# Performance work log

Measured on AMD Instinct MI355X. Metric: run time of the kernel, lower is better.

The kernel has to match this reference:

```python
import jax, jax.numpy as jnp
import numpy as np

B, Q, C, V = 512, 100, 81, 117  # batch, queries, obj classes (80+no-object), verbs
THRES, ALPHA, BETA = 0.7, 1.0, 0.5


def setup_inputs() -> dict:
    key = jax.random.key(0)
    k1, k2, k3, k4, k5, k6 = jax.random.split(key, 6)
    out_obj_logits = jax.random.normal(k1, (B, Q, C), jnp.float32)
    out_verb_logits = jax.random.normal(k2, (B, Q, V), jnp.float32)
    out_sub_boxes = jax.random.uniform(k3, (B, Q, 4), jnp.float32)
    out_obj_boxes = jax.random.uniform(k4, (B, Q, 4), jnp.float32)
    # correct_mat: binary verb-object compatibility [V, C-1] + ones column for no-object slot -> [V, C]
    cm = (jax.random.uniform(k5, (V, C - 1)) < 0.3).astype(jnp.float32)
    correct_mat = jnp.concatenate([cm, jnp.ones((V, 1), jnp.float32)], axis=1)
    target_sizes = jax.random.randint(k6, (B, 2), 480, 1334).astype(jnp.int64)
    return {
        'out_obj_logits': out_obj_logits,
        'out_verb_logits': out_verb_logits,
        'out_sub_boxes': out_sub_boxes,
        'out_obj_boxes': out_obj_boxes,
        'correct_mat': correct_mat,
        'target_sizes': target_sizes,
    }


def _box_cxcywh_to_xyxy(b):
    cx, cy, w, h = b[..., 0], b[..., 1], b[..., 2], b[..., 3]
    return jnp.stack([cx - 0.5 * w, cy - 0.5 * h, cx + 0.5 * w, cy + 0.5 * h], axis=-1)


def _pairwise_iou(boxes):  # boxes [Q,4] xyxy (pixel coords, +1 convention as in source)
    x1, y1, x2, y2 = boxes[:, 0], boxes[:, 1], boxes[:, 2], boxes[:, 3]
    area = (x2 - x1 + 1.0) * (y2 - y1 + 1.0)
    xx1 = jnp.maximum(x1[:, None], x1[None, :])
    yy1 = jnp.maximum(y1[:, None], y1[None, :])
    xx2 = jnp.minimum(x2[:, None], x2[None, :])
    yy2 = jnp.minimum(y2[:, None], y2[None, :])
    w = jnp.maximum(0.0, xx2 - xx1 + 1.0)
    h = jnp.maximum(0.0, yy2 - yy1 + 1.0)
    inter = w * h
    union = area[:, None] + area[None, :] - inter
    return inter / union


def _nms_one_image(sub_b, obj_b, obj_lab, max_scores):
    # Greedy pairwise triplet NMS. Grouping key in the source degenerates to the
    # object label alone (subject cat is constant, verb-label string identical),
    # so suppression applies only between detections with the same object label.
    order = jnp.argsort(-max_scores)
    sb, ob, lab = sub_b[order], obj_b[order], obj_lab[order]
    ovr = jnp.power(_pairwise_iou(sb), ALPHA) * jnp.power(_pairwise_iou(ob), BETA)
    upper = jnp.triu(jnp.ones((Q, Q), bool), 1)
    sup_mat = upper & (lab[:, None] == lab[None, :]) & (ovr > THRES)

    def body(i, supp):
        return supp | (sup_mat[i] & jnp.logical_not(supp[i]))

    supp = jax.lax.fori_loop(0, Q, body, jnp.zeros((Q,), bool))
    keep = jnp.zeros((Q,), bool).at[order].set(jnp.logical_not(supp))
    return keep  # in original query order


def reference(out_obj_logits, out_verb_logits, out_sub_boxes, out_obj_boxes, correct_mat, target_sizes):
    obj_prob = jax.nn.softmax(out_obj_logits, axis=-1)
    obj_scores = obj_prob[..., :-1].max(axis=-1)            # [B,Q]
    obj_labels = obj_prob[..., :-1].argmax(axis=-1)         # [B,Q]
    verb_scores = jax.nn.sigmoid(out_verb_logits)           # [B,Q,V]

    ts = target_sizes.astype(jnp.float32)
    img_h, img_w = ts[:, 0], ts[:, 1]
    scale_fct = jnp.stack([img_w, img_h, img_w, img_h], axis=1)  # [B,4]
    sub_boxes = _box_cxcywh_to_xyxy(out_sub_boxes) * scale_fct[:, None, :]
    obj_boxes = _box_cxcywh_to_xyxy(out_obj_boxes) * scale_fct[:, None, :]

    # masks[b,q,v] = correct_mat[v, obj_labels[b,q]]
    masks = correct_mat.T[obj_labels]                        # [B,Q,V]
    hoi_scores = verb_scores * obj_scores[..., None] * masks

    max_scores = hoi_scores.max(axis=-1)                     # [B,Q]
    keep = jax.vmap(_nms_one_image)(sub_boxes, obj_boxes, obj_labels, max_scores)
    return hoi_scores, obj_labels, sub_boxes, obj_boxes, keep
```

## Files before the change

### kernel.cpp

```cpp
#include <hip/hip_runtime.h>
#include <math.h>

#define Bn 512
#define Qn 100
#define Cn 81
#define Vn 117
#define NQ (Bn * Qn)

#define OFF_HOI  0
#define OFF_LAB  (NQ * Vn)
#define OFF_SUB  (OFF_LAB + NQ)
#define OFF_OBJ  (OFF_SUB + NQ * 4)
#define OFF_KEEP (OFF_OBJ + NQ * 4)

__device__ __forceinline__ float frcp(float x) { return __builtin_amdgcn_rcpf(x); }

__global__ __launch_bounds__(256) void hoi_fused(
    const float* __restrict__ obj_logits,
    const float* __restrict__ verb_logits,
    const float* __restrict__ sub_boxes,
    const float* __restrict__ obj_boxes,
    const float* __restrict__ cm,
    const int*   __restrict__ target_sizes,
    float* __restrict__ out)
{
    __shared__ float CM[Vn * Cn];
    __shared__ float L[16 * Cn];
    __shared__ float W[16 * Vn];
    __shared__ float sc[Qn];
    __shared__ int   labs[Qn];
    __shared__ float4 Bsub[Qn], Bobj[Qn];
    __shared__ float4 Ssub[Qn], Sobj[Qn], Smeta[Qn];
    __shared__ unsigned long long RR[2 * Qn];

    const int tid = threadIdx.x;
    const int b   = blockIdx.x;
    const int t   = tid & 15;
    const int g   = tid >> 4;

    {
        const float4* c4 = (const float4*)cm;
        float4* C4 = (float4*)CM;
        for (int i = tid; i < (Vn * Cn) / 4; i += 256) C4[i] = c4[i];
        if (tid == 0) CM[Vn * Cn - 1] = cm[Vn * Cn - 1];
    }

    const float ih = (float)target_sizes[2 * b + 0];
    const float iw = (float)target_sizes[2 * b + 1];

    if (tid < Qn) {
        const int idx = b * Qn + tid;
        float4 bx = ((const float4*)sub_boxes)[idx];
        float4 r;
        r.x = (bx.x - 0.5f * bx.z) * iw;
        r.y = (bx.y - 0.5f * bx.w) * ih;
        r.z = (bx.x + 0.5f * bx.z) * iw;
        r.w = (bx.y + 0.5f * bx.w) * ih;
        ((float4*)(out + OFF_SUB))[idx] = r;
        Bsub[tid] = r;
        bx = ((const float4*)obj_boxes)[idx];
        r.x = (bx.x - 0.5f * bx.z) * iw;
        r.y = (bx.y - 0.5f * bx.w) * ih;
        r.z = (bx.x + 0.5f * bx.z) * iw;
        r.w = (bx.y + 0.5f * bx.w) * ih;
        ((float4*)(out + OFF_OBJ))[idx] = r;
        Bobj[tid] = r;
    }

    for (int p = 0; p < 7; p++) {
        const int q0  = p * 16;
        const int cnt = (q0 + 16 <= Qn) ? 16 : (Qn - q0);

        {
            const float4* lgs = (const float4*)(obj_logits + ((size_t)b * Qn + q0) * Cn);
            float4* Lv = (float4*)L;
            const int nL = cnt * Cn / 4;
            for (int i = tid; i < nL; i += 256) Lv[i] = lgs[i];
            const float4* vls = (const float4*)(verb_logits + ((size_t)b * Qn + q0) * Vn);
            float4* Wv = (float4*)W;
            const int nW = cnt * Vn / 4;
            for (int i = tid; i < nW; i += 256) Wv[i] = vls[i];
        }
        __syncthreads();

        if (g < cnt) {
            const int q   = q0 + g;
            const int idx = b * Qn + q;

            const float* lg = L + g * Cn;
            float l0 = lg[t], l1 = lg[t + 16], l2 = lg[t + 32], l3 = lg[t + 48], l4 = lg[t + 64];
            float l5 = lg[80];

            float v = l0; int vid = t;
            if (l1 > v) { v = l1; vid = t + 16; }
            if (l2 > v) { v = l2; vid = t + 32; }
            if (l3 > v) { v = l3; vid = t + 48; }
            if (l4 > v) { v = l4; vid = t + 64; }
            #pragma unroll
            for (int o = 8; o; o >>= 1) {
                float ov = __shfl_xor(v, o, 64);
                int   oi = __shfl_xor(vid, o, 64);
                if (ov > v || (ov == v && oi < vid)) { v = ov; vid = oi; }
            }

            float e = __expf(l0) + __expf(l1) + __expf(l2) + __expf(l3) + __expf(l4);
            #pragma unroll
            for (int o = 8; o; o >>= 1) e += __shfl_xor(e, o, 64);
            e += __expf(l5);

            const int   label     = vid;
            const float obj_score = __expf(v) * frcp(e);

            float* vrow = W + g * Vn;
            float mx = 0.f;
            #pragma unroll
            for (int c = 0; c < 8; c++) {
                int col = t + 16 * c;
                if (col < Vn) {
                    float x = vrow[col];
                    float h = frcp(1.f + __expf(-x)) * obj_score * CM[col * Cn + label];
                    vrow[col] = h;
                    mx = fmaxf(mx, h);
                }
            }
            #pragma unroll
            for (int o = 8; o; o >>= 1) mx = fmaxf(mx, __shfl_xor(mx, o, 64));

            if (t == 0) {
                out[OFF_LAB + idx] = (float)label;
                sc[q]   = mx;
                labs[q] = label;
            }
        }
        __syncthreads();

        {
            const float4* Wv = (const float4*)W;
            float4* ho = (float4*)(out + OFF_HOI + ((size_t)b * Qn + q0) * Vn);
            const int nW = cnt * Vn / 4;
            for (int i = tid; i < nW; i += 256) ho[i] = Wv[i];
        }
        __syncthreads();
    }

    if (tid < Qn) {
        const float kv = sc[tid];
        int r = 0;
        #pragma unroll 4
        for (int j = 0; j < Qn; j++) {
            float sj = sc[j];
            r += (sj > kv) || (sj == kv && j < tid);
        }
        float4 sb = Bsub[tid], ob = Bobj[tid];
        Ssub[r] = sb;
        Sobj[r] = ob;
        Smeta[r] = make_float4((sb.z - sb.x + 1.f) * (sb.w - sb.y + 1.f),
                               (ob.z - ob.x + 1.f) * (ob.w - ob.y + 1.f),
                               (float)labs[tid], (float)tid);
    }
    __syncthreads();

    {
        const int tc   = tid & 127;
        const int half = tid >> 7;
        const int lane = tid & 63;
        const int sub  = (tid >> 6) & 1;
        const bool jv  = (tc < Qn);

        float4 js = make_float4(0.f, 0.f, 0.f, 0.f), jo = js, jm = js;
        if (jv) { js = Ssub[tc]; jo = Sobj[tc]; jm = Smeta[tc]; }

        const int i0 = half ? 50 : 0;
        const int i1 = half ? (Qn - 1) : 50;
        for (int i = i0; i < i1; i++) {
            float4 is = Ssub[i], io = Sobj[i], im = Smeta[i];
            float ww = fmaxf(0.f, fminf(is.z, js.z) - fmaxf(is.x, js.x) + 1.f);
            float hh = fmaxf(0.f, fminf(is.w, js.w) - fmaxf(is.y, js.y) + 1.f);
            float inter = ww * hh;
            float iou_s = inter / (im.x + jm.x - inter);
            ww = fmaxf(0.f, fminf(io.z, jo.z) - fmaxf(io.x, jo.x) + 1.f);
            hh = fmaxf(0.f, fminf(io.w, jo.w) - fmaxf(io.y, jo.y) + 1.f);
            inter = ww * hh;
            float iou_o = inter / (im.y + jm.y - inter);
            bool cond = jv && (tc > i) && (jm.z == im.z) && (iou_s * sqrtf(iou_o) > 0.7f);
            unsigned long long m = __ballot(cond);
            if (lane == 0) RR[2 * i + sub] = m;
        }
    }
    __syncthreads();

    if (tid < 64) {
        unsigned long long s0 = 0ull, s1 = 0ull;
        for (int k = 0; k < Qn - 1; k++) {
            unsigned long long dead = ((k < 64 ? s0 : s1) >> (k & 63)) & 1ull;
            if (!dead) { s0 |= RR[2 * k]; s1 |= RR[2 * k + 1]; }
        }
        float* keepp = out + OFF_KEEP + (size_t)b * Qn;
        keepp[(int)Smeta[tid].w] = ((s0 >> tid) & 1ull) ? 0.f : 1.f;
        if (tid < 36)
            keepp[(int)Smeta[64 + tid].w] = ((s1 >> tid) & 1ull) ? 0.f : 1.f;
    }
}

extern "C" void kernel_launch(void* const* d_in, const int* in_sizes, int n_in,
                              void* d_out, int out_size, void* d_ws, size_t ws_size,
                              hipStream_t stream) {
    const float* obj_logits   = (const float*)d_in[0];
    const float* verb_logits  = (const float*)d_in[1];
    const float* sub_boxes    = (const float*)d_in[2];
    const float* obj_boxes    = (const float*)d_in[3];
    const float* correct_mat  = (const float*)d_in[4];
    const int*   target_sizes = (const int*)d_in[5];
    float* out = (float*)d_out;
    (void)d_ws; (void)ws_size; (void)in_sizes; (void)n_in; (void)out_size;

    hoi_fused<<<Bn, 256, 0, stream>>>(obj_logits, verb_logits, sub_boxes,
                                      obj_boxes, correct_mat, target_sizes, out);
}
```

Baseline: 140.3 us.

## Read logits directly from global, drop LDS staging, use 512 threads and alias LDS

```diff
diff --git a/kernel.cpp b/kernel.cpp
--- a/kernel.cpp
+++ b/kernel.cpp
@@ -15,7 +15,7 @@
 
 __device__ __forceinline__ float frcp(float x) { return __builtin_amdgcn_rcpf(x); }
 
-__global__ __launch_bounds__(256) void hoi_fused(
+__global__ __launch_bounds__(512) void hoi_fused(
     const float* __restrict__ obj_logits,
     const float* __restrict__ verb_logits,
     const float* __restrict__ sub_boxes,
@@ -24,72 +24,59 @@
     const int*   __restrict__ target_sizes,
     float* __restrict__ out)
 {
-    __shared__ float CM[Vn * Cn];
-    __shared__ float L[16 * Cn];
-    __shared__ float W[16 * Vn];
+    __shared__ __align__(16) char smem[37920];
     __shared__ float sc[Qn];
     __shared__ int   labs[Qn];
-    __shared__ float4 Bsub[Qn], Bobj[Qn];
-    __shared__ float4 Ssub[Qn], Sobj[Qn], Smeta[Qn];
-    __shared__ unsigned long long RR[2 * Qn];
+
+    float*      CM    = (float*)smem;
+    float4*     Ssub  = (float4*)smem;
+    float4*     Sobj  = Ssub + Qn;
+    float4*     Smeta = Sobj + Qn;
+    ulonglong2* RR    = (ulonglong2*)(Smeta + Qn);
 
     const int tid = threadIdx.x;
     const int b   = blockIdx.x;
-    const int t   = tid & 15;
-    const int g   = tid >> 4;
 
     {
         const float4* c4 = (const float4*)cm;
         float4* C4 = (float4*)CM;
-        for (int i = tid; i < (Vn * Cn) / 4; i += 256) C4[i] = c4[i];
+        for (int i = tid; i < (Vn * Cn) / 4; i += 512) C4[i] = c4[i];
         if (tid == 0) CM[Vn * Cn - 1] = cm[Vn * Cn - 1];
     }
 
-    const float ih = (float)target_sizes[2 * b + 0];
-    const float iw = (float)target_sizes[2 * b + 1];
-
+    float4 rs = make_float4(0.f, 0.f, 0.f, 0.f), ro = rs;
     if (tid < Qn) {
+        const float ih = (float)target_sizes[2 * b + 0];
+        const float iw = (float)target_sizes[2 * b + 1];
         const int idx = b * Qn + tid;
         float4 bx = ((const float4*)sub_boxes)[idx];
-        float4 r;
-        r.x = (bx.x - 0.5f * bx.z) * iw;
-        r.y = (bx.y - 0.5f * bx.w) * ih;
-        r.z = (bx.x + 0.5f * bx.z) * iw;
-        r.w = (bx.y + 0.5f * bx.w) * ih;
-        ((float4*)(out + OFF_SUB))[idx] = r;
-        Bsub[tid] = r;
+        rs.x = (bx.x - 0.5f * bx.z) * iw;
+        rs.y = (bx.y - 0.5f * bx.w) * ih;
+        rs.z = (bx.x + 0.5f * bx.z) * iw;
+        rs.w = (bx.y + 0.5f * bx.w) * ih;
+        ((float4*)(out + OFF_SUB))[idx] = rs;
         bx = ((const float4*)obj_boxes)[idx];
-        r.x = (bx.x - 0.5f * bx.z) * iw;
-        r.y = (bx.y - 0.5f * bx.w) * ih;
-        r.z = (bx.x + 0.5f * bx.z) * iw;
-        r.w = (bx.y + 0.5f * bx.w) * ih;
-        ((float4*)(out + OFF_OBJ))[idx] = r;
-        Bobj[tid] = r;
-    }
-
-    for (int p = 0; p < 7; p++) {
-        const int q0  = p * 16;
-        const int cnt = (q0 + 16 <= Qn) ? 16 : (Qn - q0);
-
-        {
-            const float4* lgs = (const float4*)(obj_logits + ((size_t)b * Qn + q0) * Cn);
-            float4* Lv = (float4*)L;
-            const int nL = cnt * Cn / 4;
-            for (int i = tid; i < nL; i += 256) Lv[i] = lgs[i];
-            const float4* vls = (const float4*)(verb_logits + ((size_t)b * Qn + q0) * Vn);
-            float4* Wv = (float4*)W;
-            const int nW = cnt * Vn / 4;
-            for (int i = tid; i < nW; i += 256) Wv[i] = vls[i];
-        }
-        __syncthreads();
-
-        if (g < cnt) {
-            const int q   = q0 + g;
-            const int idx = b * Qn + q;
-
-            const float* lg = L + g * Cn;
-            float l0 = lg[t], l1 = lg[t + 16], l2 = lg[t + 32], l3 = lg[t + 48], l4 = lg[t + 64];
-            float l5 = lg[80];
+        ro.x = (bx.x - 0.5f * bx.z) * iw;
+        ro.y = (bx.y - 0.5f * bx.w) * ih;
+        ro.z = (bx.x + 0.5f * bx.z) * iw;
+        ro.w = (bx.y + 0.5f * bx.w) * ih;
+        ((float4*)(out + OFF_OBJ))[idx] = ro;
+    }
+    __syncthreads();
+
+    {
+        const int t = tid & 15;
+        const int g = tid >> 4;
+        for (int q = g; q < Qn; q += 32) {
+            const size_t idx = (size_t)b * Qn + q;
+            const float* lg = obj_logits + idx * Cn;
+            const float* vl = verb_logits + idx * Vn;
+
+            float l0 = lg[t], l1 = lg[t + 16], l2 = lg[t + 32],
+                  l3 = lg[t + 48], l4 = lg[t + 64], l5 = lg[80];
+            float w0 = vl[t], w1 = vl[t + 16], w2 = vl[t + 32], w3 = vl[t + 48],
+                  w4 = vl[t + 64], w5 = vl[t + 80], w6 = vl[t + 96];
+            float w7 = (t < 5) ? vl[112 + t] : 0.f;
 
             float v = l0; int vid = t;
             if (l1 > v) { v = l1; vid = t + 16; }
@@ -111,16 +98,28 @@
             const int   label     = vid;
             const float obj_score = __expf(v) * frcp(e);
 
-            float* vrow = W + g * Vn;
+            float* hout = out + OFF_HOI + idx * Vn;
+            const float* cmrow = CM + label;
             float mx = 0.f;
-            #pragma unroll
-            for (int c = 0; c < 8; c++) {
-                int col = t + 16 * c;
-                if (col < Vn) {
-                    float x = vrow[col];
-                    float h = frcp(1.f + __expf(-x)) * obj_score * CM[col * Cn + label];
-                    vrow[col] = h;
-                    mx = fmaxf(mx, h);
+            {
+                float h;
+                h = frcp(1.f + __expf(-w0)) * obj_score * cmrow[(t      ) * Cn];
+                hout[t      ] = h; mx = fmaxf(mx, h);
+                h = frcp(1.f + __expf(-w1)) * obj_score * cmrow[(t +  16) * Cn];
+                hout[t +  16] = h; mx = fmaxf(mx, h);
+                h = frcp(1.f + __expf(-w2)) * obj_score * cmrow[(t +  32) * Cn];
+                hout[t +  32] = h; mx = fmaxf(mx, h);
+                h = frcp(1.f + __expf(-w3)) * obj_score * cmrow[(t +  48) * Cn];
+                hout[t +  48] = h; mx = fmaxf(mx, h);
+                h = frcp(1.f + __expf(-w4)) * obj_score * cmrow[(t +  64) * Cn];
+                hout[t +  64] = h; mx = fmaxf(mx, h);
+                h = frcp(1.f + __expf(-w5)) * obj_score * cmrow[(t +  80) * Cn];
+                hout[t +  80] = h; mx = fmaxf(mx, h);
+                h = frcp(1.f + __expf(-w6)) * obj_score * cmrow[(t +  96) * Cn];
+                hout[t +  96] = h; mx = fmaxf(mx, h);
+                if (t < 5) {
+                    h = frcp(1.f + __expf(-w7)) * obj_score * cmrow[(112 + t) * Cn];
+                    hout[112 + t] = h; mx = fmaxf(mx, h);
                 }
             }
             #pragma unroll
@@ -132,16 +131,8 @@
                 labs[q] = label;
             }
         }
-        __syncthreads();
-
-        {
-            const float4* Wv = (const float4*)W;
-            float4* ho = (float4*)(out + OFF_HOI + ((size_t)b * Qn + q0) * Vn);
-            const int nW = cnt * Vn / 4;
-            for (int i = tid; i < nW; i += 256) ho[i] = Wv[i];
-        }
-        __syncthreads();
-    }
+    }
+    __syncthreads();
 
     if (tid < Qn) {
         const float kv = sc[tid];
@@ -151,18 +142,17 @@
             float sj = sc[j];
             r += (sj > kv) || (sj == kv && j < tid);
         }
-        float4 sb = Bsub[tid], ob = Bobj[tid];
-        Ssub[r] = sb;
-        Sobj[r] = ob;
-        Smeta[r] = make_float4((sb.z - sb.x + 1.f) * (sb.w - sb.y + 1.f),
-                               (ob.z - ob.x + 1.f) * (ob.w - ob.y + 1.f),
+        Ssub[r] = rs;
+        Sobj[r] = ro;
+        Smeta[r] = make_float4((rs.z - rs.x + 1.f) * (rs.w - rs.y + 1.f),
+                               (ro.z - ro.x + 1.f) * (ro.w - ro.y + 1.f),
                                (float)labs[tid], (float)tid);
     }
     __syncthreads();
 
     {
         const int tc   = tid & 127;
-        const int half = tid >> 7;
+        const int uq   = tid >> 7;
         const int lane = tid & 63;
         const int sub  = (tid >> 6) & 1;
         const bool jv  = (tc < Qn);
@@ -170,8 +160,8 @@
         float4 js = make_float4(0.f, 0.f, 0.f, 0.f), jo = js, jm = js;
         if (jv) { js = Ssub[tc]; jo = Sobj[tc]; jm = Smeta[tc]; }
 
-        const int i0 = half ? 50 : 0;
-        const int i1 = half ? (Qn - 1) : 50;
+        const int i0 = 25 * uq;
+        const int i1 = (25 * uq + 25 < Qn - 1) ? 25 * uq + 25 : Qn - 1;
         for (int i = i0; i < i1; i++) {
             float4 is = Ssub[i], io = Sobj[i], im = Smeta[i];
             float ww = fmaxf(0.f, fminf(is.z, js.z) - fmaxf(is.x, js.x) + 1.f);
@@ -184,16 +174,19 @@
             float iou_o = inter / (im.y + jm.y - inter);
             bool cond = jv && (tc > i) && (jm.z == im.z) && (iou_s * sqrtf(iou_o) > 0.7f);
             unsigned long long m = __ballot(cond);
-            if (lane == 0) RR[2 * i + sub] = m;
+            if (lane == 0) ((unsigned long long*)&RR[i])[sub] = m;
         }
     }
     __syncthreads();
 
     if (tid < 64) {
         unsigned long long s0 = 0ull, s1 = 0ull;
+        ulonglong2 r = RR[0];
         for (int k = 0; k < Qn - 1; k++) {
+            ulonglong2 rn = RR[(k + 1 < Qn - 1) ? k + 1 : k];
             unsigned long long dead = ((k < 64 ? s0 : s1) >> (k & 63)) & 1ull;
-            if (!dead) { s0 |= RR[2 * k]; s1 |= RR[2 * k + 1]; }
+            if (!dead) { s0 |= r.x; s1 |= r.y; }
+            r = rn;
         }
         float* keepp = out + OFF_KEEP + (size_t)b * Qn;
         keepp[(int)Smeta[tid].w] = ((s0 >> tid) & 1ull) ? 0.f : 1.f;
@@ -214,6 +207,6 @@
     float* out = (float*)d_out;
     (void)d_ws; (void)ws_size; (void)in_sizes; (void)n_in; (void)out_size;
 
-    hoi_fused<<<Bn, 256, 0, stream>>>(obj_logits, verb_logits, sub_boxes,
+    hoi_fused<<<Bn, 512, 0, stream>>>(obj_logits, verb_logits, sub_boxes,
                                       obj_boxes, correct_mat, target_sizes, out);
 }
```

After: 120.4 us, median of 2. 1.17x faster.
